# Kernel optimization log

Measured on AMD Instinct MI355X. Metric: run time of the kernel, lower is better.

## Reference

```python
import jax, jax.numpy as jnp
import numpy as np

S, B, E = 2048, 2, 768
H = 12
D = E // H  # 64
SCALE = D ** -0.5


def setup_inputs() -> dict:
    key = jax.random.key(0)
    ks = jax.random.split(key, 10)
    inp = {
        "query": jax.random.normal(ks[0], (S, B, E), dtype=jnp.float32),
        "attn_bias": jax.random.normal(ks[1], (B * H, S, S), dtype=jnp.float32) * 0.1,
        "key_padding_mask": jax.random.randint(ks[2], (B, S), 0, 2).astype(bool),
        "Wq": jax.random.normal(ks[3], (E, E), dtype=jnp.float32) * (E ** -0.5),
        "bq": jnp.zeros((E,), dtype=jnp.float32),
        "Wk": jax.random.normal(ks[4], (E, E), dtype=jnp.float32) * (E ** -0.5),
        "bk": jnp.zeros((E,), dtype=jnp.float32),
        "Wv": jax.random.normal(ks[5], (E, E), dtype=jnp.float32) * (E ** -0.5),
        "bv": jnp.zeros((E,), dtype=jnp.float32),
        "Wo": jax.random.normal(ks[6], (E, E), dtype=jnp.float32) * (E ** -0.5),
        "bo": jnp.zeros((E,), dtype=jnp.float32),
    }
    return inp


def reference(query, attn_bias, key_padding_mask, Wq, bq, Wk, bk, Wv, bv, Wo, bo):
    s, b, e = query.shape
    # projections (torch Linear: x @ W.T + b)
    q = (query @ Wq.T + bq) * SCALE
    k = query @ Wk.T + bk
    v = query @ Wv.T + bv
    # [s, b, e] -> [b*h, s, d]
    def to_heads(x):
        return x.reshape(s, b * H, D).transpose(1, 0, 2)
    q, k, v = to_heads(q), to_heads(k), to_heads(v)
    # scores [b*h, s_q, s_k]
    scores = jnp.einsum('nqd,nkd->nqk', q, k) + attn_bias
    # key padding mask: [b, s_k] -> broadcast over heads and queries
    scores = scores.reshape(b, H, s, s)
    scores = jnp.where(key_padding_mask[:, None, None, :], -jnp.inf, scores)
    scores = scores.reshape(b * H, s, s)
    probs = jax.nn.softmax(scores, axis=-1)
    attn = jnp.einsum('nqk,nkd->nqd', probs, v)  # [b*h, s, d]
    attn = attn.transpose(1, 0, 2).reshape(s, b, e)
    return attn @ Wo.T + bo
```

## Files before the change

kernel.cpp:

```cpp
#include <hip/hip_runtime.h>
#include <hip/hip_bf16.h>

typedef __attribute__((ext_vector_type(8))) short s16x8;
typedef __attribute__((ext_vector_type(4))) float f32x4;
typedef unsigned short u16;
typedef unsigned int u32;

#define SDIM 2048
#define BDIM 2
#define HDIM 12
#define DDIM 64
#define EDIM 768
#define MDIM 4096
#define SCALE_Q 0.125f
#define KSPLIT 1024
#define NIT (KSPLIT / 32)
#define HFRAG 131072

static __device__ __forceinline__ f32x4 zero4() {
    f32x4 v; v[0] = v[1] = v[2] = v[3] = 0.f; return v;
}

static __device__ __forceinline__ u16 f2b(float x) {
    u32 u = __builtin_bit_cast(u32, x);
    u32 lsb = (u >> 16) & 1u;
    u += 0x7fffu + lsb;
    return (u16)(u >> 16);
}

static __device__ __forceinline__ u32 cvt_pk_bf16(float lo, float hi) {
    u32 r;
    asm("v_cvt_pk_bf16_f32 %0, %1, %2" : "=v"(r) : "v"(lo), "v"(hi));
    return r;
}

static __device__ __forceinline__ f32x4 mfma16(s16x8 a, s16x8 b, f32x4 c) {
    return __builtin_amdgcn_mfma_f32_16x16x32_bf16(a, b, c, 0, 0, 0);
}

static __device__ __forceinline__ void gload_lds16(const void* g, void* l) {
    __builtin_amdgcn_global_load_lds(
        (const __attribute__((address_space(1))) void*)g,
        (__attribute__((address_space(3))) void*)l, 16, 0, 0);
}

__global__ void mask_bits_kernel(const u32* __restrict__ raw, u32* __restrict__ outbits) {
    __shared__ int okInt, okFloat;
    int t = threadIdx.x;
    if (t == 0) { okInt = 1; okFloat = 1; }
    __syncthreads();
    int li = 1, lf = 1;
    for (int i = t; i < 1024; i += blockDim.x) {
        u32 v = raw[i];
        if (v > 1u) li = 0;
        if (v != 0u && v != 0x3F800000u) lf = 0;
    }
    if (!li) atomicAnd(&okInt, 0);
    if (!lf) atomicAnd(&okFloat, 0);
    __syncthreads();
    const unsigned char* rb = (const unsigned char*)raw;
    if (t < (BDIM * SDIM) / 32) {
        u32 bits = 0;
        for (int j = 0; j < 32; ++j) {
            int i = t * 32 + j;
            int v;
            if (okInt)        v = (int)raw[i];
            else if (okFloat) v = (raw[i] != 0u) ? 1 : 0;
            else              v = (int)rb[i];
            bits |= (v ? 1u : 0u) << j;
        }
        outbits[t] = bits;
    }
}

__global__ __launch_bounds__(256) void conv_f32_bf16(
    const float* __restrict__ s, u16* __restrict__ d, int n8)
{
    int i = blockIdx.x * 256 + threadIdx.x;
    if (i >= n8) return;
    float4 x0 = ((const float4*)s)[(size_t)i * 2];
    float4 x1 = ((const float4*)s)[(size_t)i * 2 + 1];
    uint4 o;
    o.x = (u32)f2b(x0.x) | ((u32)f2b(x0.y) << 16);
    o.y = (u32)f2b(x0.z) | ((u32)f2b(x0.w) << 16);
    o.z = (u32)f2b(x1.x) | ((u32)f2b(x1.y) << 16);
    o.w = (u32)f2b(x1.z) | ((u32)f2b(x1.w) << 16);
    ((uint4*)d)[i] = o;
}

__global__ __launch_bounds__(256) void gemm_qkv(
    const u16* __restrict__ A,
    const u16* __restrict__ wq, const u16* __restrict__ wk, const u16* __restrict__ wv,
    const float* __restrict__ bq, const float* __restrict__ bk, const float* __restrict__ bv,
    u16* __restrict__ qout, u16* __restrict__ kout, u16* __restrict__ vout)
{
    __shared__ u16 Al[64 * 56];
    __shared__ u16 Bl[64 * 56];
    int tid = threadIdx.x;
    int lane = tid & 63, w = tid >> 6;
    int r16 = lane & 15, g4 = lane >> 4;
    int wm = w >> 1, wn = w & 1;
    int mb = blockIdx.x * 64;
    int nbg = blockIdx.y * 64;
    int mid = nbg / EDIM;
    int nb = nbg - mid * EDIM;
    const u16* W = (mid == 0) ? wq : (mid == 1) ? wk : wv;
    const float* bias = (mid == 0) ? bq : (mid == 1) ? bk : bv;
    float scale = (mid == 0) ? SCALE_Q : 1.0f;

    f32x4 acc[2][2];
    acc[0][0] = zero4(); acc[0][1] = zero4(); acc[1][0] = zero4(); acc[1][1] = zero4();

    int srow = tid >> 2, scol = (tid & 3) * 8;

    for (int kb = 0; kb < EDIM; kb += 32) {
        __syncthreads();
        *(uint4*)&Al[srow * 56 + scol] =
            *(const uint4*)&A[(size_t)(mb + srow) * EDIM + kb + scol];
        *(uint4*)&Bl[srow * 56 + scol] =
            *(const uint4*)&W[(size_t)(nb + srow) * EDIM + kb + scol];
        __syncthreads();
        s16x8 a[2], bb[2];
        #pragma unroll
        for (int mi = 0; mi < 2; ++mi)
            a[mi] = *(const s16x8*)&Al[(wm * 32 + mi * 16 + r16) * 56 + g4 * 8];
        #pragma unroll
        for (int ni = 0; ni < 2; ++ni)
            bb[ni] = *(const s16x8*)&Bl[(wn * 32 + ni * 16 + r16) * 56 + g4 * 8];
        #pragma unroll
        for (int mi = 0; mi < 2; ++mi)
            #pragma unroll
            for (int ni = 0; ni < 2; ++ni)
                acc[mi][ni] = mfma16(a[mi], bb[ni], acc[mi][ni]);
    }

    #pragma unroll
    for (int mi = 0; mi < 2; ++mi) {
        #pragma unroll
        for (int ni = 0; ni < 2; ++ni) {
            int n = nb + wn * 32 + ni * 16 + r16;
            float bv_ = bias[n];
            #pragma unroll
            for (int r = 0; r < 4; ++r) {
                int m = mb + wm * 32 + mi * 16 + g4 * 4 + r;
                float c = (acc[mi][ni][r] + bv_) * scale;
                int s_ = m >> 1, b_ = m & 1, h_ = n >> 6, d_ = n & 63;
                if (mid == 0) {
                    qout[((size_t)(b_ * HDIM + h_) * SDIM + s_) * DDIM + d_] = f2b(c);
                } else if (mid == 1) {
                    size_t p = (size_t)(b_ * HDIM + h_) * HFRAG
                             + (size_t)(s_ >> 4) * 1024 + (size_t)((d_ >> 5) & 1) * 512
                             + (size_t)(((d_ >> 3) & 3) * 16 + (s_ & 15)) * 8 + (d_ & 7);
                    kout[p] = f2b(c);
                } else {
                    size_t p = (size_t)(b_ * HDIM + h_) * HFRAG
                             + (size_t)(s_ >> 5) * 2048 + (size_t)((d_ >> 4) & 3) * 512
                             + (size_t)(((s_ >> 3) & 3) * 16 + (d_ & 15)) * 8 + (s_ & 7);
                    vout[p] = f2b(c);
                }
            }
        }
    }
}

__global__ __launch_bounds__(256) void gemm_out(
    const u16* __restrict__ A, const u16* __restrict__ Wb,
    const float* __restrict__ bias, float* __restrict__ out_rm)
{
    __shared__ u16 Al[64 * 56];
    __shared__ u16 Bl[64 * 56];
    int tid = threadIdx.x;
    int lane = tid & 63, w = tid >> 6;
    int r16 = lane & 15, g4 = lane >> 4;
    int wm = w >> 1, wn = w & 1;
    int mb = blockIdx.x * 64, nb = blockIdx.y * 64;

    f32x4 acc[2][2];
    acc[0][0] = zero4(); acc[0][1] = zero4(); acc[1][0] = zero4(); acc[1][1] = zero4();

    int srow = tid >> 2, scol = (tid & 3) * 8;

    for (int kb = 0; kb < EDIM; kb += 32) {
        __syncthreads();
        *(uint4*)&Al[srow * 56 + scol] =
            *(const uint4*)&A[(size_t)(mb + srow) * EDIM + kb + scol];
        *(uint4*)&Bl[srow * 56 + scol] =
            *(const uint4*)&Wb[(size_t)(nb + srow) * EDIM + kb + scol];
        __syncthreads();
        s16x8 a[2], bb[2];
        #pragma unroll
        for (int mi = 0; mi < 2; ++mi)
            a[mi] = *(const s16x8*)&Al[(wm * 32 + mi * 16 + r16) * 56 + g4 * 8];
        #pragma unroll
        for (int ni = 0; ni < 2; ++ni)
            bb[ni] = *(const s16x8*)&Bl[(wn * 32 + ni * 16 + r16) * 56 + g4 * 8];
        #pragma unroll
        for (int mi = 0; mi < 2; ++mi)
            #pragma unroll
            for (int ni = 0; ni < 2; ++ni)
                acc[mi][ni] = mfma16(a[mi], bb[ni], acc[mi][ni]);
    }

    #pragma unroll
    for (int mi = 0; mi < 2; ++mi) {
        #pragma unroll
        for (int ni = 0; ni < 2; ++ni) {
            int n = nb + wn * 32 + ni * 16 + r16;
            float bv_ = bias[n];
            #pragma unroll
            for (int r = 0; r < 4; ++r) {
                int m = mb + wm * 32 + mi * 16 + g4 * 4 + r;
                out_rm[(size_t)m * EDIM + n] = acc[mi][ni][r] + bv_;
            }
        }
    }
}

struct KV { s16x8 k0, k1, k2, k3, v0, v1, v2, v3; u32 mw; };

__global__ __launch_bounds__(128) void attn_fused(
    const u16* __restrict__ qw, const u16* __restrict__ kf_g,
    const u16* __restrict__ vf_g, const float* __restrict__ bias,
    const u32* __restrict__ maskBits, u16* __restrict__ attn_out)
{
    __shared__ __align__(1024) unsigned char SM[21504];

    int flat = blockIdx.y * 64 + blockIdx.x;
    int virt = (flat & 7) * 192 + (flat >> 3);
    int qt = virt & 63, bh = virt >> 6;

    int tid = threadIdx.x;
    int w = tid >> 6, lane = tid & 63;
    int r16 = lane & 15, g4 = lane >> 4;
    int qbase = qt * 32;
    int b_ = bh / HDIM, h_ = bh % HDIM;
    const u16* Q  = qw   + (size_t)bh * SDIM * DDIM;
    const u16* KF = kf_g + (size_t)bh * HFRAG;
    const u16* VF = vf_g + (size_t)bh * HFRAG;
    const float* BrowQ = bias + (size_t)bh * SDIM * SDIM + (size_t)qbase * SDIM;
    const u32* mB = maskBits + b_ * (SDIM / 32);

    unsigned char* wb = SM + w * 10752;
    float* RingW = (float*)wb;
    u16*   Pl    = (u16*)(wb + 8192);

    s16x8 qf[2][2];
    #pragma unroll
    for (int h = 0; h < 2; ++h) {
        qf[h][0] = *(const s16x8*)&Q[(size_t)(qbase + 16 * h + r16) * DDIM + g4 * 8];
        qf[h][1] = *(const s16x8*)&Q[(size_t)(qbase + 16 * h + r16) * DDIM + g4 * 8 + 32];
    }

    f32x4 accO[2][4];
    #pragma unroll
    for (int h = 0; h < 2; ++h)
        #pragma unroll
        for (int dt = 0; dt < 4; ++dt) accO[h][dt] = zero4();
    float m_run[2] = {-1e30f, -1e30f}, l_run[2] = {0.f, 0.f};

    const int k0 = w * KSPLIT;

    auto issue_kv = [&](int t, KV& dst) {
        int tc = t < NIT ? t : NIT - 1;
        int kbn = k0 + tc * 32;
        const u16* KT = KF + (size_t)(kbn >> 4) * 1024;
        dst.k0 = *(const s16x8*)&KT[lane * 8];
        dst.k1 = *(const s16x8*)&KT[512 + lane * 8];
        dst.k2 = *(const s16x8*)&KT[1024 + lane * 8];
        dst.k3 = *(const s16x8*)&KT[1536 + lane * 8];
        const u16* VT = VF + (size_t)(kbn >> 5) * 2048;
        dst.v0 = *(const s16x8*)&VT[lane * 8];
        dst.v1 = *(const s16x8*)&VT[512 + lane * 8];
        dst.v2 = *(const s16x8*)&VT[1024 + lane * 8];
        dst.v3 = *(const s16x8*)&VT[1536 + lane * 8];
        dst.mw = mB[kbn >> 5];
    };

    auto stage_bias = [&](int t) {
        int tc = t < NIT ? t : NIT - 1;
        int kb = k0 + tc * 32;
        unsigned char* slot = (unsigned char*)(RingW + (t & 1) * 1024);
        int sq = (lane & 7) ^ ((lane >> 3) & 7);
        #pragma unroll
        for (int j = 0; j < 4; ++j) {
            int row = j * 8 + (lane >> 3);
            gload_lds16(&BrowQ[(size_t)row * SDIM + kb + sq * 4], slot + j * 1024);
        }
    };

    auto compute = [&](int t, KV& cur) {
        u32 mw = cur.mw;
        const float* Bs = RingW + (t & 1) * 1024;
        f32x4 sc[2][2];
        #pragma unroll
        for (int h = 0; h < 2; ++h) {
            sc[h][0] = mfma16(cur.k1, qf[h][1], mfma16(cur.k0, qf[h][0], zero4()));
            sc[h][1] = mfma16(cur.k3, qf[h][1], mfma16(cur.k2, qf[h][0], zero4()));
        }
        #pragma unroll
        for (int h = 0; h < 2; ++h) {
            int rr = 16 * h + r16;
            #pragma unroll
            for (int kt = 0; kt < 2; ++kt) {
                float4 bc = *(const float4*)&Bs[rr * 32 + (((4 * kt + g4) ^ (r16 & 7)) * 4)];
                u32 mseg = (mw >> (16 * kt + 4 * g4)) & 0xF;
                sc[h][kt][0] = (mseg & 1) ? -1e30f : sc[h][kt][0] + bc.x;
                sc[h][kt][1] = (mseg & 2) ? -1e30f : sc[h][kt][1] + bc.y;
                sc[h][kt][2] = (mseg & 4) ? -1e30f : sc[h][kt][2] + bc.z;
                sc[h][kt][3] = (mseg & 8) ? -1e30f : sc[h][kt][3] + bc.w;
            }
        }
        #pragma unroll
        for (int h = 0; h < 2; ++h) {
            float pm = fmaxf(
                fmaxf(fmaxf(sc[h][0][0], sc[h][0][1]), fmaxf(sc[h][0][2], sc[h][0][3])),
                fmaxf(fmaxf(sc[h][1][0], sc[h][1][1]), fmaxf(sc[h][1][2], sc[h][1][3])));
            pm = fmaxf(pm, __shfl_xor(pm, 16));
            pm = fmaxf(pm, __shfl_xor(pm, 32));
            bool norescale = __all(pm <= m_run[h] + 4.f);
            float mn = norescale ? m_run[h] : fmaxf(m_run[h], pm);
            float p[8];
            #pragma unroll
            for (int kt = 0; kt < 2; ++kt)
                #pragma unroll
                for (int r = 0; r < 4; ++r)
                    p[kt * 4 + r] = __expf(sc[h][kt][r] - mn);
            float ps = ((p[0] + p[1]) + (p[2] + p[3])) + ((p[4] + p[5]) + (p[6] + p[7]));
            ps += __shfl_xor(ps, 16);
            ps += __shfl_xor(ps, 32);
            if (norescale) {
                l_run[h] += ps;
            } else {
                float alpha = __expf(m_run[h] - mn);
                l_run[h] = l_run[h] * alpha + ps;
                m_run[h] = mn;
                float aR0 = __shfl(alpha, g4 * 4 + 0);
                float aR1 = __shfl(alpha, g4 * 4 + 1);
                float aR2 = __shfl(alpha, g4 * 4 + 2);
                float aR3 = __shfl(alpha, g4 * 4 + 3);
                #pragma unroll
                for (int dt = 0; dt < 4; ++dt) {
                    accO[h][dt][0] *= aR0;
                    accO[h][dt][1] *= aR1;
                    accO[h][dt][2] *= aR2;
                    accO[h][dt][3] *= aR3;
                }
            }
            int rr = 16 * h + r16;
            #pragma unroll
            for (int kt = 0; kt < 2; ++kt) {
                uint2 pv;
                pv.x = cvt_pk_bf16(p[kt * 4 + 0], p[kt * 4 + 1]);
                pv.y = cvt_pk_bf16(p[kt * 4 + 2], p[kt * 4 + 3]);
                *(uint2*)&Pl[rr * 40 + kt * 16 + g4 * 4] = pv;
            }
        }
        #pragma unroll
        for (int h = 0; h < 2; ++h) {
            s16x8 pf = *(const s16x8*)&Pl[(16 * h + r16) * 40 + g4 * 8];
            accO[h][0] = mfma16(pf, cur.v0, accO[h][0]);
            accO[h][1] = mfma16(pf, cur.v1, accO[h][1]);
            accO[h][2] = mfma16(pf, cur.v2, accO[h][2]);
            accO[h][3] = mfma16(pf, cur.v3, accO[h][3]);
        }
    };

    KV A, B;
    issue_kv(0, A);
    stage_bias(0);

    for (int t = 0; t < NIT; t += 2) {
        issue_kv(t + 1, B);
        stage_bias(t + 1);
        asm volatile("s_waitcnt vmcnt(13)" ::: "memory");
        __builtin_amdgcn_sched_barrier(0);
        compute(t, A);

        issue_kv(t + 2, A);
        stage_bias(t + 2);
        asm volatile("s_waitcnt vmcnt(13)" ::: "memory");
        __builtin_amdgcn_sched_barrier(0);
        compute(t + 1, B);
    }

    __syncthreads();
    float* As = (float*)SM;
    float* Ml = (float*)(SM + 17408);
    float* Ll = Ml + 64;
    #pragma unroll
    for (int h = 0; h < 2; ++h)
        #pragma unroll
        for (int dt = 0; dt < 4; ++dt)
            #pragma unroll
            for (int r = 0; r < 4; ++r)
                As[(size_t)(w * 32 + 16 * h + g4 * 4 + r) * 68 + dt * 16 + r16] = accO[h][dt][r];
    if (g4 == 0) {
        #pragma unroll
        for (int h = 0; h < 2; ++h) {
            Ml[w * 32 + 16 * h + r16] = m_run[h];
            Ll[w * 32 + 16 * h + r16] = l_run[h];
        }
    }
    __syncthreads();

    #pragma unroll
    for (int h = 0; h < 2; ++h) {
        #pragma unroll
        for (int dg = 0; dg < 2; ++dg) {
            int d = w * 32 + dg * 16 + r16;
            #pragma unroll
            for (int r = 0; r < 4; ++r) {
                int q = 16 * h + g4 * 4 + r;
                float m0 = Ml[q], m1 = Ml[32 + q];
                float mt = fmaxf(m0, m1);
                float e0 = __expf(m0 - mt), e1 = __expf(m1 - mt);
                float lt = Ll[q] * e0 + Ll[32 + q] * e1;
                float o = (As[(size_t)q * 68 + d] * e0 + As[(size_t)(32 + q) * 68 + d] * e1) / lt;
                attn_out[((size_t)(qbase + q) * BDIM + b_) * EDIM + h_ * DDIM + d] = f2b(o);
            }
        }
    }
}

extern "C" void kernel_launch(void* const* d_in, const int* in_sizes, int n_in,
                              void* d_out, int out_size, void* d_ws, size_t ws_size,
                              hipStream_t stream) {
    const float* query     = (const float*)d_in[0];
    const float* attn_bias = (const float*)d_in[1];
    const u32*   mask_raw  = (const u32*)d_in[2];
    const float* Wq = (const float*)d_in[3];
    const float* bq = (const float*)d_in[4];
    const float* Wk = (const float*)d_in[5];
    const float* bk = (const float*)d_in[6];
    const float* Wv = (const float*)d_in[7];
    const float* bv = (const float*)d_in[8];
    const float* Wo = (const float*)d_in[9];
    const float* bo = (const float*)d_in[10];
    float* out = (float*)d_out;

    char* ws = (char*)d_ws;
    u32* maskB = (u32*)ws;
    const size_t HEADSZ = (size_t)BDIM * HDIM * SDIM * DDIM;
    const size_t WSZ = (size_t)EDIM * EDIM;
    u16* qws = (u16*)(ws + 16384);
    u16* kws = qws + HEADSZ;
    u16* vws = kws + HEADSZ;
    u16* aws = vws + HEADSZ;
    u16* qbf = aws;
    u16* wWq = aws + HEADSZ;
    u16* wWk = wWq + WSZ;
    u16* wWv = wWk + WSZ;
    u16* wWo = wWv + WSZ;

    mask_bits_kernel<<<1, 256, 0, stream>>>(mask_raw, maskB);

    conv_f32_bf16<<<(int)(MDIM * EDIM / 8 / 256), 256, 0, stream>>>(query, qbf, MDIM * EDIM / 8);
    conv_f32_bf16<<<(int)(WSZ / 8 / 256), 256, 0, stream>>>(Wq, wWq, (int)(WSZ / 8));
    conv_f32_bf16<<<(int)(WSZ / 8 / 256), 256, 0, stream>>>(Wk, wWk, (int)(WSZ / 8));
    conv_f32_bf16<<<(int)(WSZ / 8 / 256), 256, 0, stream>>>(Wv, wWv, (int)(WSZ / 8));
    conv_f32_bf16<<<(int)(WSZ / 8 / 256), 256, 0, stream>>>(Wo, wWo, (int)(WSZ / 8));

    dim3 gq(MDIM / 64, (3 * EDIM) / 64);
    gemm_qkv<<<gq, 256, 0, stream>>>(qbf, wWq, wWk, wWv, bq, bk, bv, qws, kws, vws);

    dim3 ga(64, BDIM * HDIM);
    attn_fused<<<ga, 128, 0, stream>>>(qws, kws, vws, attn_bias, maskB, aws);

    dim3 go(MDIM / 64, EDIM / 64);
    gemm_out<<<go, 256, 0, stream>>>(aws, wWo, bo, out);
}
```

Baseline: 228.6 us.

## Use single-wave attention blocks over full key range with chunked bias staging

Each attention block drops from two waves, each handling half the keys, to one wave that walks all 2048 keys. This removes the cross-wave LDS merge of partial max, sum and output, along with its two barriers. Bias tiles are now staged in 128-column chunks into a larger double-buffered LDS ring, spread across iterations. The trade-off is half as many waves per block with a serial loop twice as long, plus more LDS per block, which may lower occupancy and latency hiding.

After: 292.7 us. 1.28x slower.

```diff
diff --git a/kernel.cpp b/kernel.cpp
--- a/kernel.cpp
+++ b/kernel.cpp
@@ -13,8 +13,8 @@
 #define EDIM 768
 #define MDIM 4096
 #define SCALE_Q 0.125f
-#define KSPLIT 1024
-#define NIT (KSPLIT / 32)
+#define NBODY 64
+#define NCHUNK 16
 #define HFRAG 131072
 
 static __device__ __forceinline__ f32x4 zero4() {
@@ -218,19 +218,18 @@
 
 struct KV { s16x8 k0, k1, k2, k3, v0, v1, v2, v3; u32 mw; };
 
-__global__ __launch_bounds__(128) void attn_fused(
+__global__ __launch_bounds__(64) void attn_fused(
     const u16* __restrict__ qw, const u16* __restrict__ kf_g,
     const u16* __restrict__ vf_g, const float* __restrict__ bias,
     const u32* __restrict__ maskBits, u16* __restrict__ attn_out)
 {
-    __shared__ __align__(1024) unsigned char SM[21504];
+    __shared__ __align__(1024) unsigned char SM[35328];
 
     int flat = blockIdx.y * 64 + blockIdx.x;
     int virt = (flat & 7) * 192 + (flat >> 3);
     int qt = virt & 63, bh = virt >> 6;
 
-    int tid = threadIdx.x;
-    int w = tid >> 6, lane = tid & 63;
+    int lane = threadIdx.x;
     int r16 = lane & 15, g4 = lane >> 4;
     int qbase = qt * 32;
     int b_ = bh / HDIM, h_ = bh % HDIM;
@@ -240,9 +239,8 @@
     const float* BrowQ = bias + (size_t)bh * SDIM * SDIM + (size_t)qbase * SDIM;
     const u32* mB = maskBits + b_ * (SDIM / 32);
 
-    unsigned char* wb = SM + w * 10752;
-    float* RingW = (float*)wb;
-    u16*   Pl    = (u16*)(wb + 8192);
+    float* Ring = (float*)SM;
+    u16*   Pl   = (u16*)(SM + 32768);
 
     s16x8 qf[2][2];
     #pragma unroll
@@ -258,11 +256,9 @@
         for (int dt = 0; dt < 4; ++dt) accO[h][dt] = zero4();
     float m_run[2] = {-1e30f, -1e30f}, l_run[2] = {0.f, 0.f};
 
-    const int k0 = w * KSPLIT;
-
     auto issue_kv = [&](int t, KV& dst) {
-        int tc = t < NIT ? t : NIT - 1;
-        int kbn = k0 + tc * 32;
+        int tc = t < NBODY ? t : NBODY - 1;
+        int kbn = tc * 32;
         const u16* KT = KF + (size_t)(kbn >> 4) * 1024;
         dst.k0 = *(const s16x8*)&KT[lane * 8];
         dst.k1 = *(const s16x8*)&KT[512 + lane * 8];
@@ -273,24 +269,30 @@
         dst.v1 = *(const s16x8*)&VT[512 + lane * 8];
         dst.v2 = *(const s16x8*)&VT[1024 + lane * 8];
         dst.v3 = *(const s16x8*)&VT[1536 + lane * 8];
-        dst.mw = mB[kbn >> 5];
+        dst.mw = mB[tc];
     };
 
-    auto stage_bias = [&](int t) {
-        int tc = t < NIT ? t : NIT - 1;
-        int kb = k0 + tc * 32;
-        unsigned char* slot = (unsigned char*)(RingW + (t & 1) * 1024);
-        int sq = (lane & 7) ^ ((lane >> 3) & 7);
-        #pragma unroll
-        for (int j = 0; j < 4; ++j) {
-            int row = j * 8 + (lane >> 3);
-            gload_lds16(&BrowQ[(size_t)row * SDIM + kb + sq * 4], slot + j * 1024);
+    auto stage_part = [&](int t) {
+        int c = (t >> 2) + 1;
+        int cc = c < NCHUNK ? c : NCHUNK - 1;
+        unsigned char* slot = SM + (cc & 1) * 16384;
+        int j0 = (t & 3) * 4;
+        int half = lane >> 5;
+        int ql = lane & 31;
+        #pragma unroll
+        for (int jj = 0; jj < 4; ++jj) {
+            int j = j0 + jj;
+            int row = 2 * j + half;
+            int sq = ql ^ (row & 7);
+            gload_lds16(&BrowQ[(size_t)row * SDIM + cc * 128 + sq * 4],
+                        slot + j * 1024);
         }
     };
 
     auto compute = [&](int t, KV& cur) {
         u32 mw = cur.mw;
-        const float* Bs = RingW + (t & 1) * 1024;
+        const float* Bs = Ring + ((t >> 2) & 1) * 4096;
+        int kq0 = (t & 3) * 8;
         f32x4 sc[2][2];
         #pragma unroll
         for (int h = 0; h < 2; ++h) {
@@ -302,7 +304,8 @@
             int rr = 16 * h + r16;
             #pragma unroll
             for (int kt = 0; kt < 2; ++kt) {
-                float4 bc = *(const float4*)&Bs[rr * 32 + (((4 * kt + g4) ^ (r16 & 7)) * 4)];
+                int qd = (kq0 + kt * 4 + g4) ^ (rr & 7);
+                float4 bc = *(const float4*)&Bs[rr * 128 + qd * 4];
                 u32 mseg = (mw >> (16 * kt + 4 * g4)) & 0xF;
                 sc[h][kt][0] = (mseg & 1) ? -1e30f : sc[h][kt][0] + bc.x;
                 sc[h][kt][1] = (mseg & 2) ? -1e30f : sc[h][kt][1] + bc.y;
@@ -367,56 +370,42 @@
 
     KV A, B;
     issue_kv(0, A);
-    stage_bias(0);
-
-    for (int t = 0; t < NIT; t += 2) {
+    {
+        int half = lane >> 5, ql = lane & 31;
+        #pragma unroll
+        for (int j = 0; j < 16; ++j) {
+            int row = 2 * j + half;
+            int sq = ql ^ (row & 7);
+            gload_lds16(&BrowQ[(size_t)row * SDIM + sq * 4], SM + j * 1024);
+        }
+    }
+
+    for (int t = 0; t < NBODY; t += 2) {
         issue_kv(t + 1, B);
-        stage_bias(t + 1);
+        stage_part(t);
         asm volatile("s_waitcnt vmcnt(13)" ::: "memory");
         __builtin_amdgcn_sched_barrier(0);
         compute(t, A);
 
         issue_kv(t + 2, A);
-        stage_bias(t + 2);
+        stage_part(t + 1);
         asm volatile("s_waitcnt vmcnt(13)" ::: "memory");
         __builtin_amdgcn_sched_barrier(0);
         compute(t + 1, B);
     }
 
-    __syncthreads();
-    float* As = (float*)SM;
-    float* Ml = (float*)(SM + 17408);
-    float* Ll = Ml + 64;
-    #pragma unroll
-    for (int h = 0; h < 2; ++h)
-        #pragma unroll
-        for (int dt = 0; dt < 4; ++dt)
-            #pragma unroll
-            for (int r = 0; r < 4; ++r)
-                As[(size_t)(w * 32 + 16 * h + g4 * 4 + r) * 68 + dt * 16 + r16] = accO[h][dt][r];
-    if (g4 == 0) {
-        #pragma unroll
-        for (int h = 0; h < 2; ++h) {
-            Ml[w * 32 + 16 * h + r16] = m_run[h];
-            Ll[w * 32 + 16 * h + r16] = l_run[h];
-        }
-    }
-    __syncthreads();
-
     #pragma unroll
     for (int h = 0; h < 2; ++h) {
-        #pragma unroll
-        for (int dg = 0; dg < 2; ++dg) {
-            int d = w * 32 + dg * 16 + r16;
+        float lR[4];
+        #pragma unroll
+        for (int r = 0; r < 4; ++r) lR[r] = __shfl(l_run[h], g4 * 4 + r);
+        #pragma unroll
+        for (int dt = 0; dt < 4; ++dt) {
             #pragma unroll
             for (int r = 0; r < 4; ++r) {
                 int q = 16 * h + g4 * 4 + r;
-                float m0 = Ml[q], m1 = Ml[32 + q];
-                float mt = fmaxf(m0, m1);
-                float e0 = __expf(m0 - mt), e1 = __expf(m1 - mt);
-                float lt = Ll[q] * e0 + Ll[32 + q] * e1;
-                float o = (As[(size_t)q * 68 + d] * e0 + As[(size_t)(32 + q) * 68 + d] * e1) / lt;
-                attn_out[((size_t)(qbase + q) * BDIM + b_) * EDIM + h_ * DDIM + d] = f2b(o);
+                float o = accO[h][dt][r] / lR[r];
+                attn_out[((size_t)(qbase + q) * BDIM + b_) * EDIM + h_ * DDIM + dt * 16 + r16] = f2b(o);
             }
         }
     }
@@ -464,7 +453,7 @@
     gemm_qkv<<<gq, 256, 0, stream>>>(qbf, wWq, wWk, wWv, bq, bk, bv, qws, kws, vws);
 
     dim3 ga(64, BDIM * HDIM);
-    attn_fused<<<ga, 128, 0, stream>>>(qws, kws, vws, attn_bias, maskB, aws);
+    attn_fused<<<ga, 64, 0, stream>>>(qws, kws, vws, attn_bias, maskB, aws);
 
     dim3 go(MDIM / 64, EDIM / 64);
     gemm_out<<<go, 256, 0, stream>>>(aws, wWo, bo, out);
```

## Triple-buffer bias prefetch and pass P fragments via shuffles instead of LDS

Applied to the files above, without the earlier changes.

The bias ring grows from two slots to three so bias tiles are fetched two iterations ahead, and the vmcnt wait is loosened to match. The LDS round-trip that rearranged softmax probabilities into MFMA A-operand layout is replaced by cross-lane shuffles and selects held in registers. The goal is to hide more of the bias load latency and cut LDS write/read traffic in the inner loop. In exchange it uses more LDS per block, which may lower occupancy, adds shuffle instructions, and the vmcnt count is tuned by hand, so any mismatch would be a correctness risk.

New measurement: 223.0 us, median of 3. 2.4% less time.

```diff
diff --git a/kernel.cpp b/kernel.cpp
--- a/kernel.cpp
+++ b/kernel.cpp
@@ -223,7 +223,7 @@
     const u16* __restrict__ vf_g, const float* __restrict__ bias,
     const u32* __restrict__ maskBits, u16* __restrict__ attn_out)
 {
-    __shared__ __align__(1024) unsigned char SM[21504];
+    __shared__ __align__(1024) unsigned char SM[24576];
 
     int flat = blockIdx.y * 64 + blockIdx.x;
     int virt = (flat & 7) * 192 + (flat >> 3);
@@ -232,6 +232,7 @@
     int tid = threadIdx.x;
     int w = tid >> 6, lane = tid & 63;
     int r16 = lane & 15, g4 = lane >> 4;
+    int ga = g4 >> 1, gb = g4 & 1;
     int qbase = qt * 32;
     int b_ = bh / HDIM, h_ = bh % HDIM;
     const u16* Q  = qw   + (size_t)bh * SDIM * DDIM;
@@ -240,9 +241,11 @@
     const float* BrowQ = bias + (size_t)bh * SDIM * SDIM + (size_t)qbase * SDIM;
     const u32* mB = maskBits + b_ * (SDIM / 32);
 
-    unsigned char* wb = SM + w * 10752;
+    unsigned char* wb = SM + w * 12288;
     float* RingW = (float*)wb;
-    u16*   Pl    = (u16*)(wb + 8192);
+
+    int srcLo = (2 * gb) * 16 + r16;
+    int srcHi = (2 * gb + 1) * 16 + r16;
 
     s16x8 qf[2][2];
     #pragma unroll
@@ -279,7 +282,7 @@
     auto stage_bias = [&](int t) {
         int tc = t < NIT ? t : NIT - 1;
         int kb = k0 + tc * 32;
-        unsigned char* slot = (unsigned char*)(RingW + (t & 1) * 1024);
+        unsigned char* slot = wb + (tc % 3) * 4096;
         int sq = (lane & 7) ^ ((lane >> 3) & 7);
         #pragma unroll
         for (int j = 0; j < 4; ++j) {
@@ -290,7 +293,7 @@
 
     auto compute = [&](int t, KV& cur) {
         u32 mw = cur.mw;
-        const float* Bs = RingW + (t & 1) * 1024;
+        const float* Bs = RingW + (t % 3) * 1024;
         f32x4 sc[2][2];
         #pragma unroll
         for (int h = 0; h < 2; ++h) {
@@ -346,18 +349,20 @@
                     accO[h][dt][3] *= aR3;
                 }
             }
-            int rr = 16 * h + r16;
-            #pragma unroll
-            for (int kt = 0; kt < 2; ++kt) {
-                uint2 pv;
-                pv.x = cvt_pk_bf16(p[kt * 4 + 0], p[kt * 4 + 1]);
-                pv.y = cvt_pk_bf16(p[kt * 4 + 2], p[kt * 4 + 3]);
-                *(uint2*)&Pl[rr * 40 + kt * 16 + g4 * 4] = pv;
-            }
-        }
-        #pragma unroll
-        for (int h = 0; h < 2; ++h) {
-            s16x8 pf = *(const s16x8*)&Pl[(16 * h + r16) * 40 + g4 * 8];
+            u32 W0 = cvt_pk_bf16(p[0], p[1]);
+            u32 W1 = cvt_pk_bf16(p[2], p[3]);
+            u32 W2 = cvt_pk_bf16(p[4], p[5]);
+            u32 W3 = cvt_pk_bf16(p[6], p[7]);
+            u32 o0A = (u32)__shfl((int)W0, srcLo), o0B = (u32)__shfl((int)W2, srcLo);
+            u32 o1A = (u32)__shfl((int)W1, srcLo), o1B = (u32)__shfl((int)W3, srcLo);
+            u32 o2A = (u32)__shfl((int)W0, srcHi), o2B = (u32)__shfl((int)W2, srcHi);
+            u32 o3A = (u32)__shfl((int)W1, srcHi), o3B = (u32)__shfl((int)W3, srcHi);
+            uint4 pw;
+            pw.x = ga ? o0B : o0A;
+            pw.y = ga ? o1B : o1A;
+            pw.z = ga ? o2B : o2A;
+            pw.w = ga ? o3B : o3A;
+            s16x8 pf = __builtin_bit_cast(s16x8, pw);
             accO[h][0] = mfma16(pf, cur.v0, accO[h][0]);
             accO[h][1] = mfma16(pf, cur.v1, accO[h][1]);
             accO[h][2] = mfma16(pf, cur.v2, accO[h][2]);
@@ -368,17 +373,18 @@
     KV A, B;
     issue_kv(0, A);
     stage_bias(0);
+    stage_bias(1);
 
     for (int t = 0; t < NIT; t += 2) {
         issue_kv(t + 1, B);
-        stage_bias(t + 1);
-        asm volatile("s_waitcnt vmcnt(13)" ::: "memory");
+        stage_bias(t + 2);
+        asm volatile("s_waitcnt vmcnt(17)" ::: "memory");
         __builtin_amdgcn_sched_barrier(0);
         compute(t, A);
 
         issue_kv(t + 2, A);
-        stage_bias(t + 2);
-        asm volatile("s_waitcnt vmcnt(13)" ::: "memory");
+        stage_bias(t + 3);
+        asm volatile("s_waitcnt vmcnt(17)" ::: "memory");
         __builtin_amdgcn_sched_barrier(0);
         compute(t + 1, B);
     }
```
